# Kernel tuning notes

Measured on AMD Instinct MI355X. Metric: run time of the kernel, lower is better.

Reference implementation:

```python
import jax, jax.numpy as jnp
import numpy as np

BETA = 0.95
THR = 1.0
T = 50        # NUM_TIME_STEPS
L = 2         # SNN_NUM_LAYERS
SLOPE = 25.0  # fast_sigmoid surrogate slope

@jax.custom_vjp
def spike(v):
    # Heaviside on (mem - threshold) with fast_sigmoid surrogate gradient
    return (v > 0).astype(v.dtype)

def _spike_fwd(v):
    return (v > 0).astype(v.dtype), v

def _spike_bwd(v, g):
    return (g / (SLOPE * jnp.abs(v) + 1.0) ** 2,)

spike.defvjp(_spike_fwd, _spike_bwd)


def setup_inputs() -> dict:
    key = jax.random.key(0)
    k1, k2, _ = jax.random.split(key, 3)
    B, IN, H = 4096, 512, 1024
    x = jax.random.normal(k1, (B, IN), dtype=jnp.float32)
    W_proj = jax.random.normal(k2, (IN, H), dtype=jnp.float32) / np.sqrt(IN).astype(np.float32)
    b_proj = jnp.zeros((H,), dtype=jnp.float32)
    return {"x": x, "W_proj": W_proj, "b_proj": b_proj}


def reference(x, W_proj, b_proj):
    # Static input current fed at every time step (input_features != hidden -> Linear projection)
    inp = x @ W_proj + b_proj                         # [B, H]
    B, H = inp.shape

    def step(carry, _):
        mems, agg, tot = carry
        new_mems = []
        for li in range(L):  # independent LIF layers, all driven by the same static input
            mem = mems[li]
            # snnTorch Leaky (reset_mechanism='subtract'):
            reset = spike(mem - THR)                  # reset based on previous mem
            mem = BETA * mem + inp - reset * THR      # leaky integration + subtractive reset
            spk = spike(mem - THR)                    # output spike from new mem
            new_mems.append(mem)
            tot = tot + spk.sum(axis=1)               # total spikes per sample (all layers)
            if li == L - 1:
                agg = agg + spk                       # sum of last-layer spikes over time
        return (tuple(new_mems), agg, tot), None

    init = (
        tuple(jnp.zeros((B, H), inp.dtype) for _ in range(L)),  # init_leaky -> zeros
        jnp.zeros((B, H), inp.dtype),
        jnp.zeros((B,), inp.dtype),
    )
    (mems, agg, tot), _ = jax.lax.scan(step, init, None, length=T)
    return agg, tot
```

## Files before the change

kernel.cpp:

```cpp
#include <hip/hip_runtime.h>
#include <stdint.h>

#define MDIM 4096
#define NDIM 1024
#define KDIM 512
#define TSTEPS 50
#define NCH 24

typedef _Float16 half8 __attribute__((ext_vector_type(8)));
typedef float    f32x4 __attribute__((ext_vector_type(4)));

typedef const __attribute__((address_space(1))) void cgv_t;
typedef __attribute__((address_space(3))) void lv_t;

__device__ __forceinline__ void gload16(const void* g, void* s) {
    __builtin_amdgcn_global_load_lds((cgv_t*)g, (lv_t*)s, 16, 0, 0);
}


__global__ __launch_bounds__(256) void asplit_kernel(
    const float* __restrict__ A, _Float16* __restrict__ A1,
    _Float16* __restrict__ A2, float* __restrict__ tot)
{
    int idx = blockIdx.x * 256 + threadIdx.x;
    if (idx < MDIM) tot[idx] = 0.0f;
    int r = idx >> 6, k8 = idx & 63;
    float4 v0 = *(const float4*)(A + (size_t)r * KDIM + k8 * 8);
    float4 v1 = *(const float4*)(A + (size_t)r * KDIM + k8 * 8 + 4);
    float v[8] = {v0.x, v0.y, v0.z, v0.w, v1.x, v1.y, v1.z, v1.w};
    half8 h1, h2;
    #pragma unroll
    for (int e = 0; e < 8; ++e) {
        h1[e] = (_Float16)v[e];
        h2[e] = (_Float16)((v[e] - (float)h1[e]) * 2048.0f);
    }
    int off = r * 1024 + (k8 >> 3) * 128 + (((k8 & 7) * 16) ^ ((r & 7) << 4));
    *(half8*)((char*)A1 + off) = h1;
    *(half8*)((char*)A2 + off) = h2;
}

__global__ __launch_bounds__(256) void wsplit_kernel(
    const float* __restrict__ W, _Float16* __restrict__ B1, _Float16* __restrict__ B2)
{
    int idx = blockIdx.x * 256 + threadIdx.x;
    int n = idx >> 6, k8 = idx & 63;
    float v[8];
    #pragma unroll
    for (int e = 0; e < 8; ++e) v[e] = W[(size_t)(k8 * 8 + e) * NDIM + n];
    half8 h1, h2;
    #pragma unroll
    for (int e = 0; e < 8; ++e) {
        h1[e] = (_Float16)v[e];
        h2[e] = (_Float16)((v[e] - (float)h1[e]) * 2048.0f);
    }
    int off = n * 1024 + (k8 >> 3) * 128 + (((k8 & 7) * 16) ^ ((n & 7) << 4));
    *(half8*)((char*)B1 + off) = h1;
    *(half8*)((char*)B2 + off) = h2;
}

__global__ __launch_bounds__(256, 4) void snn_mfma_kernel(
    const _Float16* __restrict__ A1, const _Float16* __restrict__ A2,
    const _Float16* __restrict__ B1, const _Float16* __restrict__ B2,
    const float* __restrict__ bias, float* __restrict__ agg, float* __restrict__ tot)
{
    __shared__ __align__(16) unsigned char lds[2][16384];

    const int t  = threadIdx.x;
    const int l  = t & 63;
    const int w  = t >> 6;
    const int li = l & 15;
    const int lg = l >> 4;
    const int qr = (w >> 1) * 32;
    const int qc = (w & 1) * 32;

    const int swz = (blockIdx.x & 7) * 128 + (blockIdx.x >> 3);
    const int m0 = (swz >> 4) * 64;
    const int n0 = (swz & 15) * 64;

    int aoff[2], boff[2], dstA[2], dstB[2];
    #pragma unroll
    for (int i_ = 0; i_ < 2; ++i_) {
        int rr  = i_ * 32 + w * 8 + (l >> 3);
        aoff[i_] = (m0 + rr) * 1024 + (l & 7) * 16;
        boff[i_] = (n0 + rr) * 1024 + (l & 7) * 16;
        dstA[i_] = (i_ * 32 + w * 8) * 128;
        dstB[i_] = 8192 + (i_ * 32 + w * 8) * 128;
    }

#define STAGE(buf, ch) do {                                                   \
    const int seg_ = (ch) >> 3, c_ = ((ch) & 7) * 128;                        \
    const char* As_ = (const char*)((seg_ == 0) ? A2 : A1);                   \
    const char* Bs_ = (const char*)((seg_ == 1) ? B2 : B1);                   \
    _Pragma("unroll") for (int i_ = 0; i_ < 2; ++i_)                          \
        gload16(As_ + aoff[i_] + c_, &lds[buf][dstA[i_]]);                    \
    _Pragma("unroll") for (int i_ = 0; i_ < 2; ++i_)                          \
        gload16(Bs_ + boff[i_] + c_, &lds[buf][dstB[i_]]);                    \
} while (0)

    f32x4 acc[2][2];
    #pragma unroll
    for (int i = 0; i < 2; ++i)
        #pragma unroll
        for (int j = 0; j < 2; ++j) acc[i][j] = (f32x4){0.f, 0.f, 0.f, 0.f};

    STAGE(0, 0);
    STAGE(1, 1);

    #pragma unroll 1
    for (int ch = 0; ch < NCH; ++ch) {
        if (ch < NCH - 1) asm volatile("s_waitcnt vmcnt(4)" ::: "memory");
        else              asm volatile("s_waitcnt vmcnt(0)" ::: "memory");
        __builtin_amdgcn_s_barrier();
        asm volatile("" ::: "memory");
        const unsigned char* sAb = &lds[ch & 1][0];
        const unsigned char* sBb = &lds[ch & 1][8192];
        #pragma unroll
        for (int ks = 0; ks < 2; ++ks) {
            const int kb = ks * 64 + lg * 16;
            half8 af[2], bf[2];
            #pragma unroll
            for (int i = 0; i < 2; ++i) {
                const int r_ = qr + i * 16 + li;
                af[i] = *(const half8*)(sAb + r_ * 128 + (kb ^ ((r_ & 7) << 4)));
            }
            #pragma unroll
            for (int j = 0; j < 2; ++j) {
                const int c_ = qc + j * 16 + li;
                bf[j] = *(const half8*)(sBb + c_ * 128 + (kb ^ ((c_ & 7) << 4)));
            }
            #pragma unroll
            for (int i = 0; i < 2; ++i)
                #pragma unroll
                for (int j = 0; j < 2; ++j)
                    acc[i][j] = __builtin_amdgcn_mfma_f32_16x16x32_f16(
                        af[i], bf[j], acc[i][j], 0, 0, 0);
        }
        if (ch == 15) {
            #pragma unroll
            for (int i = 0; i < 2; ++i)
                #pragma unroll
                for (int j = 0; j < 2; ++j)
                    acc[i][j] *= (1.0f / 2048.0f);
        }
        __builtin_amdgcn_s_barrier();
        asm volatile("" ::: "memory");
        if (ch + 2 < NCH) STAGE(ch & 1, ch + 2);
    }

    float cb[2];
    #pragma unroll
    for (int j = 0; j < 2; ++j) cb[j] = bias[n0 + qc + j * 16 + li];

    #pragma unroll
    for (int i = 0; i < 2; ++i) {
        int rsum[4] = {0, 0, 0, 0};
        #pragma unroll
        for (int j = 0; j < 2; ++j) {
            float c[4], c1[4], mem[4];
            int cnt[4];
            bool sp[4];
            #pragma unroll
            for (int r = 0; r < 4; ++r) {
                c[r]   = acc[i][j][r] + cb[j];
                c1[r]  = c[r] - 1.0f;
                mem[r] = 0.0f;
                cnt[r] = 0;
                sp[r]  = false;
            }
            #pragma unroll 1
            for (int tt = 0; tt < TSTEPS; ++tt) {
                #pragma unroll
                for (int r = 0; r < 4; ++r) {
                    mem[r] = fmaf(0.95f, mem[r], sp[r] ? c1[r] : c[r]);
                    sp[r]  = mem[r] > 1.0f;
                    cnt[r] += sp[r] ? 1 : 0;
                }
            }
            const int col = n0 + qc + j * 16 + li;
            #pragma unroll
            for (int r = 0; r < 4; ++r) {
                const int row = m0 + qr + i * 16 + lg * 4 + r;
                agg[(size_t)row * NDIM + col] = (float)cnt[r];
                rsum[r] += cnt[r];
            }
        }
        #pragma unroll
        for (int r = 0; r < 4; ++r) {
            int s = rsum[r];
            s += __shfl_xor(s, 1);
            s += __shfl_xor(s, 2);
            s += __shfl_xor(s, 4);
            s += __shfl_xor(s, 8);
            if (li == 0)
                atomicAdd(&tot[m0 + qr + i * 16 + lg * 4 + r], 2.0f * (float)s);
        }
        __builtin_amdgcn_sched_barrier(0);
    }
}

extern "C" void kernel_launch(void* const* d_in, const int* in_sizes, int n_in,
                              void* d_out, int out_size, void* d_ws, size_t ws_size,
                              hipStream_t stream) {
    const float* x = (const float*)d_in[0];
    const float* W = (const float*)d_in[1];
    const float* b = (const float*)d_in[2];
    float* agg = (float*)d_out;
    float* tot = agg + (size_t)MDIM * NDIM;

    char* ws = (char*)d_ws;
    _Float16* A1 = (_Float16*)(ws);
    _Float16* A2 = (_Float16*)(ws + (4 << 20));
    _Float16* B1 = (_Float16*)(ws + (8 << 20));
    _Float16* B2 = (_Float16*)(ws + (9 << 20));

    asplit_kernel<<<(MDIM * KDIM / 8) / 256, 256, 0, stream>>>(x, A1, A2, tot);
    wsplit_kernel<<<(NDIM * KDIM / 8) / 256, 256, 0, stream>>>(W, B1, B2);
    snn_mfma_kernel<<<(MDIM / 64) * (NDIM / 64), 256, 0, stream>>>(
        A1, A2, B1, B2, b, agg, tot);
}
```

Before: 59.55 us.

## Triple-buffer LDS pipeline, drop second barrier, and merge split kernels

The GEMM main loop moves from two to three LDS buffers. This lets the prefetch for chunk ch+2 be issued right after the single per-chunk barrier, so the trailing barrier can be removed. MFMA sections are wrapped in s_setprio to favour the math waves. The two fp16 split preprocessing kernels are merged into one launch to cut launch overhead. The larger LDS footprint lowers the occupancy target from 4 to 3 blocks per CU.

```diff
diff --git a/kernel.cpp b/kernel.cpp
--- a/kernel.cpp
+++ b/kernel.cpp
@@ -17,53 +17,53 @@
     __builtin_amdgcn_global_load_lds((cgv_t*)g, (lv_t*)s, 16, 0, 0);
 }
 
-
-__global__ __launch_bounds__(256) void asplit_kernel(
-    const float* __restrict__ A, _Float16* __restrict__ A1,
-    _Float16* __restrict__ A2, float* __restrict__ tot)
+__global__ __launch_bounds__(256) void split_kernel(
+    const float* __restrict__ A, const float* __restrict__ W,
+    _Float16* __restrict__ A1, _Float16* __restrict__ A2,
+    _Float16* __restrict__ B1, _Float16* __restrict__ B2,
+    float* __restrict__ tot)
 {
-    int idx = blockIdx.x * 256 + threadIdx.x;
-    if (idx < MDIM) tot[idx] = 0.0f;
-    int r = idx >> 6, k8 = idx & 63;
-    float4 v0 = *(const float4*)(A + (size_t)r * KDIM + k8 * 8);
-    float4 v1 = *(const float4*)(A + (size_t)r * KDIM + k8 * 8 + 4);
-    float v[8] = {v0.x, v0.y, v0.z, v0.w, v1.x, v1.y, v1.z, v1.w};
-    half8 h1, h2;
-    #pragma unroll
-    for (int e = 0; e < 8; ++e) {
-        h1[e] = (_Float16)v[e];
-        h2[e] = (_Float16)((v[e] - (float)h1[e]) * 2048.0f);
-    }
-    int off = r * 1024 + (k8 >> 3) * 128 + (((k8 & 7) * 16) ^ ((r & 7) << 4));
-    *(half8*)((char*)A1 + off) = h1;
-    *(half8*)((char*)A2 + off) = h2;
-}
-
-__global__ __launch_bounds__(256) void wsplit_kernel(
-    const float* __restrict__ W, _Float16* __restrict__ B1, _Float16* __restrict__ B2)
-{
-    int idx = blockIdx.x * 256 + threadIdx.x;
-    int n = idx >> 6, k8 = idx & 63;
-    float v[8];
-    #pragma unroll
-    for (int e = 0; e < 8; ++e) v[e] = W[(size_t)(k8 * 8 + e) * NDIM + n];
-    half8 h1, h2;
-    #pragma unroll
-    for (int e = 0; e < 8; ++e) {
-        h1[e] = (_Float16)v[e];
-        h2[e] = (_Float16)((v[e] - (float)h1[e]) * 2048.0f);
-    }
-    int off = n * 1024 + (k8 >> 3) * 128 + (((k8 & 7) * 16) ^ ((n & 7) << 4));
-    *(half8*)((char*)B1 + off) = h1;
-    *(half8*)((char*)B2 + off) = h2;
-}
-
-__global__ __launch_bounds__(256, 4) void snn_mfma_kernel(
+    const int blk = blockIdx.x;
+    if (blk < 1024) {
+        int idx = blk * 256 + threadIdx.x;
+        if (idx < MDIM) tot[idx] = 0.0f;
+        int r = idx >> 6, k8 = idx & 63;
+        float4 v0 = *(const float4*)(A + (size_t)r * KDIM + k8 * 8);
+        float4 v1 = *(const float4*)(A + (size_t)r * KDIM + k8 * 8 + 4);
+        float v[8] = {v0.x, v0.y, v0.z, v0.w, v1.x, v1.y, v1.z, v1.w};
+        half8 h1, h2;
+        #pragma unroll
+        for (int e = 0; e < 8; ++e) {
+            h1[e] = (_Float16)v[e];
+            h2[e] = (_Float16)((v[e] - (float)h1[e]) * 2048.0f);
+        }
+        int off = r * 1024 + (k8 >> 3) * 128 + (((k8 & 7) * 16) ^ ((r & 7) << 4));
+        *(half8*)((char*)A1 + off) = h1;
+        *(half8*)((char*)A2 + off) = h2;
+    } else {
+        int idx = (blk - 1024) * 256 + threadIdx.x;
+        int n = idx >> 6, k8 = idx & 63;
+        float v[8];
+        #pragma unroll
+        for (int e = 0; e < 8; ++e) v[e] = W[(size_t)(k8 * 8 + e) * NDIM + n];
+        half8 h1, h2;
+        #pragma unroll
+        for (int e = 0; e < 8; ++e) {
+            h1[e] = (_Float16)v[e];
+            h2[e] = (_Float16)((v[e] - (float)h1[e]) * 2048.0f);
+        }
+        int off = n * 1024 + (k8 >> 3) * 128 + (((k8 & 7) * 16) ^ ((n & 7) << 4));
+        *(half8*)((char*)B1 + off) = h1;
+        *(half8*)((char*)B2 + off) = h2;
+    }
+}
+
+__global__ __launch_bounds__(256, 3) void snn_mfma_kernel(
     const _Float16* __restrict__ A1, const _Float16* __restrict__ A2,
     const _Float16* __restrict__ B1, const _Float16* __restrict__ B2,
     const float* __restrict__ bias, float* __restrict__ agg, float* __restrict__ tot)
 {
-    __shared__ __align__(16) unsigned char lds[2][16384];
+    __shared__ __align__(16) unsigned char lds[3][16384];
 
     const int t  = threadIdx.x;
     const int l  = t & 63;
@@ -106,14 +106,19 @@
     STAGE(0, 0);
     STAGE(1, 1);
 
+    int bcur = 0, bst = 2;
+
     #pragma unroll 1
     for (int ch = 0; ch < NCH; ++ch) {
         if (ch < NCH - 1) asm volatile("s_waitcnt vmcnt(4)" ::: "memory");
         else              asm volatile("s_waitcnt vmcnt(0)" ::: "memory");
         __builtin_amdgcn_s_barrier();
         asm volatile("" ::: "memory");
-        const unsigned char* sAb = &lds[ch & 1][0];
-        const unsigned char* sBb = &lds[ch & 1][8192];
+        if (ch + 2 < NCH) STAGE(bst, ch + 2);
+
+        const unsigned char* sAb = &lds[bcur][0];
+        const unsigned char* sBb = &lds[bcur][8192];
+        __builtin_amdgcn_s_setprio(1);
         #pragma unroll
         for (int ks = 0; ks < 2; ++ks) {
             const int kb = ks * 64 + lg * 16;
@@ -135,6 +140,7 @@
                     acc[i][j] = __builtin_amdgcn_mfma_f32_16x16x32_f16(
                         af[i], bf[j], acc[i][j], 0, 0, 0);
         }
+        __builtin_amdgcn_s_setprio(0);
         if (ch == 15) {
             #pragma unroll
             for (int i = 0; i < 2; ++i)
@@ -142,9 +148,8 @@
                 for (int j = 0; j < 2; ++j)
                     acc[i][j] *= (1.0f / 2048.0f);
         }
-        __builtin_amdgcn_s_barrier();
-        asm volatile("" ::: "memory");
-        if (ch + 2 < NCH) STAGE(ch & 1, ch + 2);
+        bcur = (bcur == 2) ? 0 : bcur + 1;
+        bst  = (bst  == 2) ? 0 : bst  + 1;
     }
 
     float cb[2];
@@ -213,8 +218,7 @@
     _Float16* B1 = (_Float16*)(ws + (8 << 20));
     _Float16* B2 = (_Float16*)(ws + (9 << 20));
 
-    asplit_kernel<<<(MDIM * KDIM / 8) / 256, 256, 0, stream>>>(x, A1, A2, tot);
-    wsplit_kernel<<<(NDIM * KDIM / 8) / 256, 256, 0, stream>>>(W, B1, B2);
+    split_kernel<<<1024 + 256, 256, 0, stream>>>(x, W, A1, A2, B1, B2, tot);
     snn_mfma_kernel<<<(MDIM / 64) * (NDIM / 64), 256, 0, stream>>>(
         A1, A2, B1, B2, b, agg, tot);
 }
```

Result: slower. 63.36 us (+6.4%).
